# Kernel optimization log

Measured on AMD Instinct MI355X. Metric: run time of the kernel, lower is better.

## Reference

```python
import jax, jax.numpy as jnp
import numpy as np

NSAMPLE = 64  # init kwarg nsample
BN_EPS = 1e-5


def setup_inputs() -> dict:
    key = jax.random.key(0)
    ks = jax.random.split(key, 8)
    B, N = 8, 4096
    C_IN, NC = 6, 3
    NP = 1024
    M = [64, 64, 128]
    C0 = C_IN + NC
    xyz = jax.random.normal(ks[0], (B, 3, N), dtype=jnp.float32)
    points = jax.random.normal(ks[1], (B, C_IN, N), dtype=jnp.float32)
    one_hot_vec = jax.nn.one_hot(jax.random.randint(ks[2], (B,), 0, NC), NC, dtype=jnp.float32)
    idx = jax.random.randint(ks[3], (B, NP), 0, N, dtype=jnp.int64)
    w1 = jax.random.normal(ks[4], (M[0], C0), dtype=jnp.float32) * (1.0 / np.sqrt(C0))
    w2 = jax.random.normal(ks[5], (M[1], M[0]), dtype=jnp.float32) * (1.0 / np.sqrt(M[0]))
    w3 = jax.random.normal(ks[6], (M[2], M[1]), dtype=jnp.float32) * (1.0 / np.sqrt(M[1]))
    g1, b1 = jnp.ones((M[0],), jnp.float32), jnp.zeros((M[0],), jnp.float32)
    g2, b2 = jnp.ones((M[1],), jnp.float32), jnp.zeros((M[1],), jnp.float32)
    g3, b3 = jnp.ones((M[2],), jnp.float32), jnp.zeros((M[2],), jnp.float32)
    return {"xyz": xyz, "points": points, "one_hot_vec": one_hot_vec, "idx": idx,
            "w1": w1, "g1": g1, "b1": b1, "w2": w2, "g2": g2, "b2": b2,
            "w3": w3, "g3": g3, "b3": b3}


def _conv_bn_relu(x, w, gamma, beta):
    # x: (B, C, NP, NS); w: (O, C) -- 1x1 conv, no bias; BN with batch stats (train mode)
    y = jnp.einsum('oc,bcpn->bopn', w, x)
    mu = jnp.mean(y, axis=(0, 2, 3), keepdims=True)
    var = jnp.var(y, axis=(0, 2, 3), keepdims=True)
    y = (y - mu) * jax.lax.rsqrt(var + BN_EPS)
    y = y * gamma[None, :, None, None] + beta[None, :, None, None]
    return jax.nn.relu(y)


def reference(xyz, points, one_hot_vec, idx, w1, g1, b1, w2, g2, b2, w3, g3, b3):
    B, _, N = xyz.shape
    NP = idx.shape[1]
    NS = NSAMPLE
    # concat one-hot class vector onto per-point features: (B, C_in + NC, N)
    feat = jnp.concatenate(
        [points, jnp.broadcast_to(one_hot_vec[:, :, None], (B, one_hot_vec.shape[1], N))], axis=1)
    C = feat.shape[1]
    # gather sampled centers; idx is repeated nsample times in the original,
    # so every sample slot holds the center itself -> broadcast along NS
    gathered = jnp.take_along_axis(feat, idx[:, None, :], axis=2)          # (B, C, NP)
    grouped_points = jnp.broadcast_to(gathered[..., None], (B, C, NP, NS))  # (B, C, NP, NS)
    cx = jnp.take_along_axis(xyz, idx[:, None, :], axis=2)                 # (B, 3, NP)
    cxt = jnp.transpose(cx, (0, 2, 1))[:, :, None, :]                      # (B, NP, 1, 3)
    grouped_xyz = jnp.broadcast_to(cxt - cxt, (B, NP, NS, 3))              # zeros (center-relative)
    # pointwise conv-BN-ReLU MLP, then max over the nsample axis
    x = _conv_bn_relu(grouped_points, w1, g1, b1)
    x = _conv_bn_relu(x, w2, g2, b2)
    x = _conv_bn_relu(x, w3, g3, b3)
    pooled = jnp.max(x, axis=3)  # (B, mlp[-1], NP)
    return grouped_xyz, pooled
```

## Files before the change

### kernel.cpp

```cpp
#include <hip/hip_runtime.h>

constexpr int B    = 8;
constexpr int N    = 4096;
constexpr int CIN  = 6;
constexpr int NC   = 3;
constexpr int NP   = 1024;
constexpr int C0   = CIN + NC;
constexpr int M1   = 64;
constexpr int M2   = 64;
constexpr int M3   = 128;
constexpr int NPTS = B * NP;
constexpr float EPS = 1e-5f;

constexpr int GZ_ELEMS = B * NP * 64 * 3;
constexpr size_t Y1_OFF = 0;
constexpr size_t Y2_OFF = Y1_OFF + (size_t)M1 * NPTS;
constexpr size_t Y3_OFF = Y2_OFF + (size_t)M2 * NPTS;
constexpr size_t AB1_OFF = Y3_OFF + (size_t)M3 * NPTS;
constexpr size_t AB2_OFF = AB1_OFF + 2 * M1;
constexpr size_t AB3_OFF = AB2_OFF + 2 * M2;

constexpr int OC1 = 8;
__global__ void k_gather_l1(const float* __restrict__ points,
                            const float* __restrict__ onehot,
                            const int* __restrict__ idx,
                            const float* __restrict__ w1,
                            float* __restrict__ y1) {
    constexpr int NOB = M1 / OC1;
    __shared__ float ws[OC1 * C0];
    int t = threadIdx.x;
    int ob = blockIdx.x % NOB;
    int pb = blockIdx.x / NOB;
    int o0 = ob * OC1;
    if (t < OC1 * C0) ws[t] = w1[o0 * C0 + t];
    __syncthreads();

    int p  = pb * blockDim.x + t;
    int b  = p >> 10;
    int pp = p & (NP - 1);
    int n  = idx[b * NP + pp];

    float f[C0];
#pragma unroll
    for (int c = 0; c < CIN; ++c) f[c] = points[((size_t)b * CIN + c) * N + n];
#pragma unroll
    for (int c = 0; c < NC; ++c)  f[CIN + c] = onehot[b * NC + c];

#pragma unroll
    for (int o = 0; o < OC1; ++o) {
        float acc = 0.f;
#pragma unroll
        for (int c = 0; c < C0; ++c) acc += ws[o * C0 + c] * f[c];
        y1[(size_t)(o0 + o) * NPTS + p] = acc;
    }
}

__device__ inline void block_reduce2(float& s, float& s2) {
    for (int off = 32; off; off >>= 1) {
        s  += __shfl_down(s,  off, 64);
        s2 += __shfl_down(s2, off, 64);
    }
    __shared__ float ls[4], ls2[4];
    int lane = threadIdx.x & 63;
    int w    = threadIdx.x >> 6;
    if (lane == 0) { ls[w] = s; ls2[w] = s2; }
    __syncthreads();
    if (threadIdx.x == 0) {
        for (int i = 1; i < 4; ++i) { s += ls[i]; s2 += ls2[i]; }
    }
}

__global__ void k_stats(const float* __restrict__ y,
                        const float* __restrict__ gamma,
                        const float* __restrict__ beta,
                        float* __restrict__ AB) {
    int c = blockIdx.x;
    const float4* yc4 = (const float4*)(y + (size_t)c * NPTS);
    float s = 0.f, s2 = 0.f;
#pragma unroll
    for (int i = threadIdx.x; i < NPTS / 4; i += 256) {
        float4 v = yc4[i];
        s  += v.x + v.y + v.z + v.w;
        s2 += v.x * v.x + v.y * v.y + v.z * v.z + v.w * v.w;
    }
    block_reduce2(s, s2);
    if (threadIdx.x == 0) {
        float inv_n = 1.0f / (float)NPTS;
        float mean = s * inv_n;
        float var  = s2 * inv_n - mean * mean;
        float istd = rsqrtf(var + EPS);
        float A = gamma[c] * istd;
        float Bb = beta[c] - mean * A;
        AB[2 * c]     = A;
        AB[2 * c + 1] = Bb;
    }
}

template <int CI, int CO, int OC>
__global__ void k_mlp(const float* __restrict__ yin,
                      const float* __restrict__ AB,
                      const float* __restrict__ w,
                      float* __restrict__ yout) {
    constexpr int NOB = CO / OC;
    __shared__ float ws[OC * CI];
    __shared__ float sAB[2 * CI];
    int t = threadIdx.x;
    int ob = blockIdx.x % NOB;
    int pb = blockIdx.x / NOB;
    int o0 = ob * OC;
    for (int i = t; i < OC * CI; i += blockDim.x) ws[i] = w[o0 * CI + i];
    if (t < 2 * CI) sAB[t] = AB[t];
    __syncthreads();

    int p = pb * blockDim.x + t;

    float x[CI];
#pragma unroll
    for (int c = 0; c < CI; ++c) {
        float v = yin[(size_t)c * NPTS + p] * sAB[2 * c] + sAB[2 * c + 1];
        x[c] = v > 0.f ? v : 0.f;
    }
#pragma unroll
    for (int o = 0; o < OC; ++o) {
        float acc = 0.f;
#pragma unroll
        for (int c = 0; c < CI; ++c) acc += ws[o * CI + c] * x[c];
        yout[(size_t)(o0 + o) * NPTS + p] = acc;
    }
}

__global__ void k_out(const float* __restrict__ y3,
                      const float* __restrict__ AB,
                      float* __restrict__ out) {
    int gid = blockIdx.x * blockDim.x + threadIdx.x;
    int e0  = gid * 4;
    int pp  = e0 & (NP - 1);
    int c   = (e0 >> 10) & (M3 - 1);
    int b   = e0 >> 17;
    float A  = AB[2 * c];
    float Bb = AB[2 * c + 1];
    const float4 v = *(const float4*)(y3 + (size_t)c * NPTS + b * NP + pp);
    float4 r;
    r.x = fmaxf(v.x * A + Bb, 0.f);
    r.y = fmaxf(v.y * A + Bb, 0.f);
    r.z = fmaxf(v.z * A + Bb, 0.f);
    r.w = fmaxf(v.w * A + Bb, 0.f);
    *(float4*)(out + e0) = r;
}

extern "C" void kernel_launch(void* const* d_in, const int* in_sizes, int n_in,
                              void* d_out, int out_size, void* d_ws, size_t ws_size,
                              hipStream_t stream) {
    const float* points = (const float*)d_in[1];
    const float* onehot = (const float*)d_in[2];
    const int*   idx    = (const int*)d_in[3];
    const float* w1 = (const float*)d_in[4];
    const float* g1 = (const float*)d_in[5];
    const float* b1 = (const float*)d_in[6];
    const float* w2 = (const float*)d_in[7];
    const float* g2 = (const float*)d_in[8];
    const float* b2 = (const float*)d_in[9];
    const float* w3 = (const float*)d_in[10];
    const float* g3 = (const float*)d_in[11];
    const float* b3 = (const float*)d_in[12];

    float* out = (float*)d_out;
    float* ws  = (float*)d_ws;
    float* y1  = ws + Y1_OFF;
    float* y2  = ws + Y2_OFF;
    float* y3  = ws + Y3_OFF;
    float* AB1 = ws + AB1_OFF;
    float* AB2 = ws + AB2_OFF;
    float* AB3 = ws + AB3_OFF;

    hipMemsetAsync(d_out, 0, (size_t)GZ_ELEMS * sizeof(float), stream);

    const int T = 256;
    const int PBLK = NPTS / T;

    k_gather_l1<<<(M1 / OC1) * PBLK, T, 0, stream>>>(points, onehot, idx, w1, y1);
    k_stats<<<M1, T, 0, stream>>>(y1, g1, b1, AB1);
    k_mlp<M1, M2, 8><<<(M2 / 8) * PBLK, T, 0, stream>>>(y1, AB1, w2, y2);
    k_stats<<<M2, T, 0, stream>>>(y2, g2, b2, AB2);
    k_mlp<M2, M3, 8><<<(M3 / 8) * PBLK, T, 0, stream>>>(y2, AB2, w3, y3);
    k_stats<<<M3, T, 0, stream>>>(y3, g3, b3, AB3);
    k_out<<<(B * M3 * NP / 4) / T, T, 0, stream>>>(y3, AB3, out + GZ_ELEMS);
}
```

Before: 43.64 us.

## Fuse BN statistics into producer kernels and fold memset into gather

Each conv kernel now emits per-block partial sums and sums of squares for its output channels. The consumer kernel folds these partials into BN scale and shift at block start, which removes the three separate stats kernels that re-read each activation buffer. The zeroing of grouped_xyz moves from a memset into the first kernel, and k_out is restructured to one row per block with a per-channel fold. This cuts launches and memory re-reads, at the cost of each block redundantly summing 32 partials per channel.

Measured after the change: 37.02 us. 1.18x faster.

```diff
diff --git a/kernel.cpp b/kernel.cpp
--- a/kernel.cpp
+++ b/kernel.cpp
@@ -10,22 +10,77 @@
 constexpr int M2   = 64;
 constexpr int M3   = 128;
 constexpr int NPTS = B * NP;
+constexpr int NPB  = NPTS / 256;
 constexpr float EPS = 1e-5f;
 
 constexpr int GZ_ELEMS = B * NP * 64 * 3;
+constexpr int GZ_F4    = GZ_ELEMS / 4;
 constexpr size_t Y1_OFF = 0;
 constexpr size_t Y2_OFF = Y1_OFF + (size_t)M1 * NPTS;
 constexpr size_t Y3_OFF = Y2_OFF + (size_t)M2 * NPTS;
-constexpr size_t AB1_OFF = Y3_OFF + (size_t)M3 * NPTS;
-constexpr size_t AB2_OFF = AB1_OFF + 2 * M1;
-constexpr size_t AB3_OFF = AB2_OFF + 2 * M2;
+constexpr size_t PS1_OFF = Y3_OFF + (size_t)M3 * NPTS;
+constexpr size_t PQ1_OFF = PS1_OFF + (size_t)M1 * NPB;
+constexpr size_t PS2_OFF = PQ1_OFF + (size_t)M1 * NPB;
+constexpr size_t PQ2_OFF = PS2_OFF + (size_t)M2 * NPB;
+constexpr size_t PS3_OFF = PQ2_OFF + (size_t)M2 * NPB;
+constexpr size_t PQ3_OFF = PS3_OFF + (size_t)M3 * NPB;
+
+template <int OC>
+__device__ inline void emit_partials(const float (&acc)[OC], int o0, int pb,
+                                     float* __restrict__ ps, float* __restrict__ pq) {
+    float sv[OC], qv[OC];
+#pragma unroll
+    for (int o = 0; o < OC; ++o) { sv[o] = acc[o]; qv[o] = acc[o] * acc[o]; }
+#pragma unroll
+    for (int off = 32; off; off >>= 1) {
+#pragma unroll
+        for (int o = 0; o < OC; ++o) {
+            sv[o] += __shfl_down(sv[o], off, 64);
+            qv[o] += __shfl_down(qv[o], off, 64);
+        }
+    }
+    __shared__ float rs[OC][4], rq[OC][4];
+    int lane = threadIdx.x & 63, w = threadIdx.x >> 6;
+    if (lane == 0) {
+#pragma unroll
+        for (int o = 0; o < OC; ++o) { rs[o][w] = sv[o]; rq[o][w] = qv[o]; }
+    }
+    __syncthreads();
+    if (threadIdx.x < OC) {
+        int o = threadIdx.x;
+        float s = rs[o][0] + rs[o][1] + rs[o][2] + rs[o][3];
+        float q = rq[o][0] + rq[o][1] + rq[o][2] + rq[o][3];
+        ps[(o0 + o) * NPB + pb] = s;
+        pq[(o0 + o) * NPB + pb] = q;
+    }
+}
+
+template <int CI>
+__device__ inline void fold_AB(const float* __restrict__ ps, const float* __restrict__ pq,
+                               const float* __restrict__ gamma, const float* __restrict__ beta,
+                               float* __restrict__ sAB) {
+    int t = threadIdx.x;
+    if (t < CI) {
+        float s = 0.f, q = 0.f;
+#pragma unroll 8
+        for (int i = 0; i < NPB; ++i) { s += ps[t * NPB + i]; q += pq[t * NPB + i]; }
+        float inv_n = 1.0f / (float)NPTS;
+        float mean = s * inv_n;
+        float var  = q * inv_n - mean * mean;
+        float A = gamma[t] * rsqrtf(var + EPS);
+        sAB[2 * t]     = A;
+        sAB[2 * t + 1] = beta[t] - mean * A;
+    }
+}
 
 constexpr int OC1 = 8;
-__global__ void k_gather_l1(const float* __restrict__ points,
-                            const float* __restrict__ onehot,
-                            const int* __restrict__ idx,
-                            const float* __restrict__ w1,
-                            float* __restrict__ y1) {
+__global__ void k1_gather(const float* __restrict__ points,
+                          const float* __restrict__ onehot,
+                          const int* __restrict__ idx,
+                          const float* __restrict__ w1,
+                          float* __restrict__ y1,
+                          float* __restrict__ ps1, float* __restrict__ pq1,
+                          float4* __restrict__ gz) {
     constexpr int NOB = M1 / OC1;
     __shared__ float ws[OC1 * C0];
     int t = threadIdx.x;
@@ -33,9 +88,17 @@
     int pb = blockIdx.x / NOB;
     int o0 = ob * OC1;
     if (t < OC1 * C0) ws[t] = w1[o0 * C0 + t];
-    __syncthreads();
-
-    int p  = pb * blockDim.x + t;
+
+    {
+        constexpr int PER_BLK = GZ_F4 / (NOB * NPB);
+        float4 z = make_float4(0.f, 0.f, 0.f, 0.f);
+        float4* g = gz + (size_t)blockIdx.x * PER_BLK + t;
+#pragma unroll
+        for (int i = 0; i < PER_BLK / 256; ++i) g[i * 256] = z;
+    }
+    __syncthreads();
+
+    int p  = pb * 256 + t;
     int b  = p >> 10;
     int pp = p & (NP - 1);
     int n  = idx[b * NP + pp];
@@ -46,61 +109,25 @@
 #pragma unroll
     for (int c = 0; c < NC; ++c)  f[CIN + c] = onehot[b * NC + c];
 
+    float acc[OC1];
 #pragma unroll
     for (int o = 0; o < OC1; ++o) {
-        float acc = 0.f;
-#pragma unroll
-        for (int c = 0; c < C0; ++c) acc += ws[o * C0 + c] * f[c];
-        y1[(size_t)(o0 + o) * NPTS + p] = acc;
-    }
-}
-
-__device__ inline void block_reduce2(float& s, float& s2) {
-    for (int off = 32; off; off >>= 1) {
-        s  += __shfl_down(s,  off, 64);
-        s2 += __shfl_down(s2, off, 64);
-    }
-    __shared__ float ls[4], ls2[4];
-    int lane = threadIdx.x & 63;
-    int w    = threadIdx.x >> 6;
-    if (lane == 0) { ls[w] = s; ls2[w] = s2; }
-    __syncthreads();
-    if (threadIdx.x == 0) {
-        for (int i = 1; i < 4; ++i) { s += ls[i]; s2 += ls2[i]; }
-    }
-}
-
-__global__ void k_stats(const float* __restrict__ y,
-                        const float* __restrict__ gamma,
-                        const float* __restrict__ beta,
-                        float* __restrict__ AB) {
-    int c = blockIdx.x;
-    const float4* yc4 = (const float4*)(y + (size_t)c * NPTS);
-    float s = 0.f, s2 = 0.f;
-#pragma unroll
-    for (int i = threadIdx.x; i < NPTS / 4; i += 256) {
-        float4 v = yc4[i];
-        s  += v.x + v.y + v.z + v.w;
-        s2 += v.x * v.x + v.y * v.y + v.z * v.z + v.w * v.w;
-    }
-    block_reduce2(s, s2);
-    if (threadIdx.x == 0) {
-        float inv_n = 1.0f / (float)NPTS;
-        float mean = s * inv_n;
-        float var  = s2 * inv_n - mean * mean;
-        float istd = rsqrtf(var + EPS);
-        float A = gamma[c] * istd;
-        float Bb = beta[c] - mean * A;
-        AB[2 * c]     = A;
-        AB[2 * c + 1] = Bb;
-    }
+        float a = 0.f;
+#pragma unroll
+        for (int c = 0; c < C0; ++c) a += ws[o * C0 + c] * f[c];
+        acc[o] = a;
+        y1[(size_t)(o0 + o) * NPTS + p] = a;
+    }
+    emit_partials<OC1>(acc, o0, pb, ps1, pq1);
 }
 
 template <int CI, int CO, int OC>
 __global__ void k_mlp(const float* __restrict__ yin,
-                      const float* __restrict__ AB,
+                      const float* __restrict__ psin, const float* __restrict__ pqin,
+                      const float* __restrict__ gamma, const float* __restrict__ beta,
                       const float* __restrict__ w,
-                      float* __restrict__ yout) {
+                      float* __restrict__ yout,
+                      float* __restrict__ psout, float* __restrict__ pqout) {
     constexpr int NOB = CO / OC;
     __shared__ float ws[OC * CI];
     __shared__ float sAB[2 * CI];
@@ -108,44 +135,60 @@
     int ob = blockIdx.x % NOB;
     int pb = blockIdx.x / NOB;
     int o0 = ob * OC;
-    for (int i = t; i < OC * CI; i += blockDim.x) ws[i] = w[o0 * CI + i];
-    if (t < 2 * CI) sAB[t] = AB[t];
-    __syncthreads();
-
-    int p = pb * blockDim.x + t;
-
+
+    fold_AB<CI>(psin, pqin, gamma, beta, sAB);
+    for (int i = t; i < OC * CI; i += 256) ws[i] = w[o0 * CI + i];
+    __syncthreads();
+
+    int p = pb * 256 + t;
     float x[CI];
 #pragma unroll
     for (int c = 0; c < CI; ++c) {
         float v = yin[(size_t)c * NPTS + p] * sAB[2 * c] + sAB[2 * c + 1];
         x[c] = v > 0.f ? v : 0.f;
     }
+    float acc[OC];
 #pragma unroll
     for (int o = 0; o < OC; ++o) {
-        float acc = 0.f;
-#pragma unroll
-        for (int c = 0; c < CI; ++c) acc += ws[o * CI + c] * x[c];
-        yout[(size_t)(o0 + o) * NPTS + p] = acc;
-    }
+        float a = 0.f;
+#pragma unroll
+        for (int c = 0; c < CI; ++c) a += ws[o * CI + c] * x[c];
+        acc[o] = a;
+        yout[(size_t)(o0 + o) * NPTS + p] = a;
+    }
+    __syncthreads();
+    emit_partials<OC>(acc, o0, pb, psout, pqout);
 }
 
 __global__ void k_out(const float* __restrict__ y3,
-                      const float* __restrict__ AB,
+                      const float* __restrict__ ps, const float* __restrict__ pq,
+                      const float* __restrict__ gamma, const float* __restrict__ beta,
                       float* __restrict__ out) {
-    int gid = blockIdx.x * blockDim.x + threadIdx.x;
-    int e0  = gid * 4;
-    int pp  = e0 & (NP - 1);
-    int c   = (e0 >> 10) & (M3 - 1);
-    int b   = e0 >> 17;
-    float A  = AB[2 * c];
-    float Bb = AB[2 * c + 1];
-    const float4 v = *(const float4*)(y3 + (size_t)c * NPTS + b * NP + pp);
+    int row = blockIdx.x;
+    int c = row & (M3 - 1);
+    int b = row >> 7;
+    __shared__ float sA, sB;
+    int t = threadIdx.x;
+    if (t == 0) {
+        float s = 0.f, q = 0.f;
+#pragma unroll 8
+        for (int i = 0; i < NPB; ++i) { s += ps[c * NPB + i]; q += pq[c * NPB + i]; }
+        float inv_n = 1.0f / (float)NPTS;
+        float mean = s * inv_n;
+        float var  = q * inv_n - mean * mean;
+        float A = gamma[c] * rsqrtf(var + EPS);
+        sA = A;
+        sB = beta[c] - mean * A;
+    }
+    __syncthreads();
+    float A = sA, Bb = sB;
+    const float4 v = ((const float4*)(y3 + (size_t)c * NPTS + b * NP))[t];
     float4 r;
     r.x = fmaxf(v.x * A + Bb, 0.f);
     r.y = fmaxf(v.y * A + Bb, 0.f);
     r.z = fmaxf(v.z * A + Bb, 0.f);
     r.w = fmaxf(v.w * A + Bb, 0.f);
-    *(float4*)(out + e0) = r;
+    ((float4*)(out + (size_t)row * NP))[t] = r;
 }
 
 extern "C" void kernel_launch(void* const* d_in, const int* in_sizes, int n_in,
@@ -169,20 +212,17 @@
     float* y1  = ws + Y1_OFF;
     float* y2  = ws + Y2_OFF;
     float* y3  = ws + Y3_OFF;
-    float* AB1 = ws + AB1_OFF;
-    float* AB2 = ws + AB2_OFF;
-    float* AB3 = ws + AB3_OFF;
-
-    hipMemsetAsync(d_out, 0, (size_t)GZ_ELEMS * sizeof(float), stream);
+    float* ps1 = ws + PS1_OFF;  float* pq1 = ws + PQ1_OFF;
+    float* ps2 = ws + PS2_OFF;  float* pq2 = ws + PQ2_OFF;
+    float* ps3 = ws + PS3_OFF;  float* pq3 = ws + PQ3_OFF;
 
     const int T = 256;
-    const int PBLK = NPTS / T;
-
-    k_gather_l1<<<(M1 / OC1) * PBLK, T, 0, stream>>>(points, onehot, idx, w1, y1);
-    k_stats<<<M1, T, 0, stream>>>(y1, g1, b1, AB1);
-    k_mlp<M1, M2, 8><<<(M2 / 8) * PBLK, T, 0, stream>>>(y1, AB1, w2, y2);
-    k_stats<<<M2, T, 0, stream>>>(y2, g2, b2, AB2);
-    k_mlp<M2, M3, 8><<<(M3 / 8) * PBLK, T, 0, stream>>>(y2, AB2, w3, y3);
-    k_stats<<<M3, T, 0, stream>>>(y3, g3, b3, AB3);
-    k_out<<<(B * M3 * NP / 4) / T, T, 0, stream>>>(y3, AB3, out + GZ_ELEMS);
-}
+
+    k1_gather<<<(M1 / OC1) * NPB, T, 0, stream>>>(points, onehot, idx, w1,
+                                                  y1, ps1, pq1, (float4*)d_out);
+    k_mlp<M1, M2, 8><<<(M2 / 8) * NPB, T, 0, stream>>>(y1, ps1, pq1, g1, b1, w2,
+                                                       y2, ps2, pq2);
+    k_mlp<M2, M3, 8><<<(M3 / 8) * NPB, T, 0, stream>>>(y2, ps2, pq2, g2, b2, w3,
+                                                       y3, ps3, pq3);
+    k_out<<<B * M3, T, 0, stream>>>(y3, ps3, pq3, g3, b3, out + GZ_ELEMS);
+}
```
